# Optimization experiments

Hardware: AMD Instinct MI355X
Metric: run time of the kernel (lower is better)

The kernel has to match this reference:

```python
import jax, jax.numpy as jnp
import numpy as np

ALPHA = 0.2  # LeakyReLU negative slope
NEG_INF = -9e15


def setup_inputs() -> dict:
    key = jax.random.key(0)
    k1, k2, k3, k4 = jax.random.split(key, 4)
    B, N, F_in, F_out = 8, 2048, 256, 128
    h = jax.random.normal(k1, (B, N, F_in), dtype=jnp.float32)
    adj = jax.random.randint(k2, (B, N, N), 0, 2, dtype=jnp.int32)
    # xavier_uniform with gain=1.414
    def xavier(k, shape, gain=1.414):
        fan_in, fan_out = shape[0], shape[1]
        limit = gain * np.sqrt(6.0 / (fan_in + fan_out))
        return jax.random.uniform(k, shape, jnp.float32, -limit, limit)
    W = xavier(k3, (F_in, F_out))
    a = xavier(k4, (2 * F_out, 1))
    return {"h": h, "adj": adj, "W": W, "a": a}


def reference(h, adj, W, a):
    # h: [B,N,F_in], adj: [B,N,N], W: [F_in,F_out], a: [2*F_out,1]
    Wh = jnp.einsum('bnf,fe->bne', h, W)  # [B,N,E]
    E = Wh.shape[-1]
    a_src, a_dst = a[:E, 0], a[E:, 0]
    # e[b,i,j] = leakyrelu(Wh[b,i].a_src + Wh[b,j].a_dst)  (additive decomposition
    # of a @ concat(Wh_i, Wh_j) -- same math, no [B,N,N,2E] intermediate)
    s_src = Wh @ a_src  # [B,N]
    s_dst = Wh @ a_dst  # [B,N]
    e = jax.nn.leaky_relu(s_src[:, :, None] + s_dst[:, None, :], negative_slope=ALPHA)
    e = jnp.where(adj > 0, e, NEG_INF)
    attention = jax.nn.softmax(e, axis=2)  # [B,N,N]
    # dropout p=0.0 / eval mode -> identity
    h_prime = jnp.einsum('bij,bje->bie', attention, Wh)
    return jax.nn.elu(h_prime)  # concat=True
```

## Files before the change

kernel.cpp:

```cpp
#include <hip/hip_runtime.h>
#include <hip/hip_bf16.h>

#define GAT_ALPHA 0.2f
#define LOG2E 1.4426950408889634f

typedef float f32x4 __attribute__((ext_vector_type(4)));
typedef int   i32x4 __attribute__((ext_vector_type(4)));
typedef short bf16x8 __attribute__((ext_vector_type(8)));

static constexpr int Nn  = 2048;
static constexpr int FIN = 256;
static constexpr int FO  = 128;

static __device__ __forceinline__ unsigned short f2bf(float x) {
    __hip_bfloat16 h = __float2bfloat16(x);
    return __builtin_bit_cast(unsigned short, h);
}
static __device__ __forceinline__ float bf2f(unsigned short u) {
    unsigned int v = ((unsigned int)u) << 16;
    return __builtin_bit_cast(float, v);
}

__global__ __launch_bounds__(256) void gat_prep(
        const float* __restrict__ W, const float* __restrict__ a,
        float* __restrict__ wa, unsigned int* __restrict__ md_key)
{
    __shared__ float pr[32][8];
    __shared__ float pd[32][8];
    const int t = threadIdx.x;
    const int kl = t >> 3, seg = t & 7;
    const int k = blockIdx.x * 32 + kl;
    float ps = 0.f, pv = 0.f;
    const float* wr = W + (size_t)k * FO + seg * 16;
    #pragma unroll
    for (int f = 0; f < 16; f += 4) {
        f32x4 wv = *(const f32x4*)(wr + f);
        f32x4 as = *(const f32x4*)(a + seg * 16 + f);
        f32x4 ad = *(const f32x4*)(a + FO + seg * 16 + f);
        ps += wv[0]*as[0] + wv[1]*as[1] + wv[2]*as[2] + wv[3]*as[3];
        pv += wv[0]*ad[0] + wv[1]*ad[1] + wv[2]*ad[2] + wv[3]*ad[3];
    }
    pr[kl][seg] = ps; pd[kl][seg] = pv;
    __syncthreads();
    if (t < 32) {
        float s = 0.f, d = 0.f;
        #pragma unroll
        for (int j = 0; j < 8; ++j) { s += pr[t][j]; d += pd[t][j]; }
        wa[blockIdx.x * 32 + t]       = s;
        wa[256 + blockIdx.x * 32 + t] = d;
    }
    if (blockIdx.x == 0 && t < 8) md_key[t] = 0u;
}

__global__ __launch_bounds__(256) void gat_pack(
        const int* __restrict__ adj, unsigned int* __restrict__ mask)
{
    const int t = threadIdx.x, lane = t & 63, w = t >> 6;
    const size_t ibase = ((size_t)blockIdx.x * 4 + w) * 2048;
    const int* src = adj + ibase + lane;
    unsigned int myword = 0;
    #pragma unroll
    for (int c = 0; c < 32; ++c) {
        int v = src[(size_t)c * 64];
        unsigned long long m = __ballot(v > 0);
        if (lane == 2 * c)     myword = (unsigned int)m;
        if (lane == 2 * c + 1) myword = (unsigned int)(m >> 32);
    }
    mask[ibase / 32 + lane] = myword;
}

__global__ __launch_bounds__(256) void gat_wh(
        const float* __restrict__ h, const float* __restrict__ W,
        const float* __restrict__ wa, unsigned short* __restrict__ Wp,
        float* __restrict__ s_src, float* __restrict__ s_dst,
        unsigned int* __restrict__ md_key)
{
    __shared__ unsigned short WT[FO][264];
    __shared__ float wal[512];
    __shared__ float sred[64][4][2];
    __shared__ float red64[64];
    const int t  = threadIdx.x;
    const int b  = blockIdx.x & 7;
    const int n0 = (blockIdx.x >> 3) << 6;

    if (t < 128) *(f32x4*)&wal[t * 4] = *(const f32x4*)&wa[t * 4];
    #pragma unroll
    for (int c = 0; c < 32; ++c) {
        int flat = c * 1024 + t * 4;
        int k = flat >> 7, f = flat & 127;
        f32x4 wv = *(const f32x4*)&W[flat];
        WT[f + 0][k] = f2bf(wv[0]);
        WT[f + 1][k] = f2bf(wv[1]);
        WT[f + 2][k] = f2bf(wv[2]);
        WT[f + 3][k] = f2bf(wv[3]);
    }
    __syncthreads();

    {
        const int row = t >> 2, seg = t & 3;
        const float* hp  = h + ((size_t)(b * Nn + n0 + row)) * FIN + seg * 64;
        const float* was = &wal[seg * 64];
        const float* wad = &wal[256 + seg * 64];
        float ps = 0.f, pv = 0.f;
        #pragma unroll
        for (int j = 0; j < 64; j += 4) {
            f32x4 hv = *(const f32x4*)(hp + j);
            f32x4 sv = *(const f32x4*)(was + j);
            f32x4 dv = *(const f32x4*)(wad + j);
            ps += hv[0]*sv[0] + hv[1]*sv[1] + hv[2]*sv[2] + hv[3]*sv[3];
            pv += hv[0]*dv[0] + hv[1]*dv[1] + hv[2]*dv[2] + hv[3]*dv[3];
        }
        sred[row][seg][0] = ps;
        sred[row][seg][1] = pv;
    }
    __syncthreads();
    if (t < 64) {
        float s = sred[t][0][0] + sred[t][1][0] + sred[t][2][0] + sred[t][3][0];
        float d = sred[t][0][1] + sred[t][1][1] + sred[t][2][1] + sred[t][3][1];
        s_src[b * Nn + n0 + t] = s;
        s_dst[b * Nn + n0 + t] = d;
        red64[t] = d;
    }
    __syncthreads();
    if (t < 16) red64[t] = fmaxf(fmaxf(red64[t], red64[t + 16]),
                                 fmaxf(red64[t + 32], red64[t + 48]));
    __syncthreads();
    if (t == 0) {
        float m = red64[0];
        #pragma unroll
        for (int j = 1; j < 16; ++j) m = fmaxf(m, red64[j]);
        unsigned int bits = __builtin_bit_cast(unsigned int, m);
        unsigned int key  = (bits & 0x80000000u) ? ~bits : (bits | 0x80000000u);
        atomicMax(md_key + b, key);
    }

    const int w = t >> 6, lane = t & 63, n16 = lane & 15, quad = lane >> 4;
    const float* ha = h + ((size_t)(b * Nn + n0 + w * 16 + n16)) * FIN + quad * 8;
    f32x4 acc[8] = {};
    #pragma unroll
    for (int ks = 0; ks < 8; ++ks) {
        f32x4 h0 = *(const f32x4*)(ha + ks * 32);
        f32x4 h1 = *(const f32x4*)(ha + ks * 32 + 4);
        bf16x8 af;
        af[0] = (short)f2bf(h0[0]); af[1] = (short)f2bf(h0[1]);
        af[2] = (short)f2bf(h0[2]); af[3] = (short)f2bf(h0[3]);
        af[4] = (short)f2bf(h1[0]); af[5] = (short)f2bf(h1[1]);
        af[6] = (short)f2bf(h1[2]); af[7] = (short)f2bf(h1[3]);
        #pragma unroll
        for (int nt = 0; nt < 8; ++nt) {
            bf16x8 bfr = *(const bf16x8*)&WT[nt * 16 + n16][ks * 32 + quad * 8];
            acc[nt] = __builtin_amdgcn_mfma_f32_16x16x32_bf16(af, bfr, acc[nt], 0, 0, 0);
        }
    }
    {
        const int v      = (n0 >> 5) + (w >> 1);
        const int quad_p = ((w & 1) << 1) + (quad >> 1);
        const int eoff   = (quad & 1) << 2;
        #pragma unroll
        for (int nt = 0; nt < 8; ++nt) {
            ushort4 pk;
            pk.x = f2bf(acc[nt][0]); pk.y = f2bf(acc[nt][1]);
            pk.z = f2bf(acc[nt][2]); pk.w = f2bf(acc[nt][3]);
            size_t idx = ((((size_t)(b << 6) + v) * 8 + nt) * 64 + quad_p * 16 + n16) * 8 + eoff;
            *(ushort4*)&Wp[idx] = pk;
        }
    }
}

__global__ __launch_bounds__(512, 2) void gat_attn(
        const unsigned int* __restrict__ mask, const unsigned short* __restrict__ Wp,
        const float* __restrict__ s_src, const float* __restrict__ s_dst,
        const unsigned int* __restrict__ md_key, float* __restrict__ out)
{
    constexpr int AS = 132;
    constexpr int MS = 68;
    __shared__ __align__(16) float smem_f[64 * AS];
    __shared__ __align__(16) unsigned int mlds[64 * MS];
    __shared__ __align__(16) float dlds[Nn];
    __shared__ float l_red[64];
    unsigned short* ldsw = (unsigned short*)smem_f;

    const int t = threadIdx.x, w = t >> 6, lane = t & 63;
    const int n16 = lane & 15, quad = lane >> 4;
    const int rg = w & 3, jwin = w >> 2;
    const int b  = blockIdx.x & 7;
    const int i0 = (blockIdx.x >> 3) << 6;

    if (t < 64) l_red[t] = 0.f;

    {
        const unsigned int* msrc = mask + ((size_t)(b * Nn + i0)) * 64 + t * 8;
        i32x4 m0 = *(const i32x4*)(msrc);
        i32x4 m1 = *(const i32x4*)(msrc + 4);
        const int r = t >> 3, wd = (t & 7) * 8;
        *(i32x4*)&mlds[r * MS + wd]     = m0;
        *(i32x4*)&mlds[r * MS + wd + 4] = m1;
    }
    {
        f32x4 dv = *(const f32x4*)(s_dst + b * Nn + t * 4);
        *(f32x4*)&dlds[t * 4] = dv;
    }

    const unsigned int key = md_key[b];
    const unsigned int mb  = (key & 0x80000000u) ? (key ^ 0x80000000u) : ~key;
    const float mdb = __builtin_bit_cast(float, mb);

    const int row = i0 + rg * 16 + n16;
    const float ssr = s_src[b * Nn + row];
    const float tm  = ssr + mdb;
    const float mi  = fmaxf(tm, GAT_ALPHA * tm) * LOG2E;
    const float sL  = ssr * LOG2E;

    const int jw = (jwin << 5) + (quad << 3);
    const int mrow = (rg * 16 + n16) * MS;
    const unsigned short* wsrc = Wp + ((size_t)b << 18) + (t << 4);

    f32x4 acc[8] = {};
    float ls = 0.f;

    {
        f32x4 g0 = *(const f32x4*)(wsrc);
        f32x4 g1 = *(const f32x4*)(wsrc + 8);
        *(f32x4*)&ldsw[(t << 4)]     = g0;
        *(f32x4*)&ldsw[(t << 4) + 8] = g1;
    }
    __syncthreads();

    for (int s = 0; s < 32; ++s) {
        const int j0  = s << 6;
        const int cur = s & 1, nxt = cur ^ 1;
        const unsigned int mword = mlds[mrow + s * 2 + jwin];
        const unsigned int mbyte = (mword >> (quad * 8)) & 0xffu;
        f32x4 d0 = *(const f32x4*)&dlds[j0 + jw];
        f32x4 d1 = *(const f32x4*)&dlds[j0 + jw + 4];
        f32x4 g0, g1;
        if (s < 31) {
            const unsigned short* src = wsrc + (size_t)(s + 1) * 8192;
            g0 = *(const f32x4*)(src);
            g1 = *(const f32x4*)(src + 8);
        }

        bf16x8 af;
        #pragma unroll
        for (int j = 0; j < 4; ++j) {
            float u  = __builtin_fmaf(d0[j], LOG2E, sL);
            float lr = fmaxf(u, GAT_ALPHA * u);
            float e  = __builtin_amdgcn_exp2f(lr - mi);
            e = ((mbyte >> j) & 1u) ? e : 0.f;
            unsigned short us = f2bf(e);
            ls += bf2f(us); af[j] = (short)us;
        }
        #pragma unroll
        for (int j = 0; j < 4; ++j) {
            float u  = __builtin_fmaf(d1[j], LOG2E, sL);
            float lr = fmaxf(u, GAT_ALPHA * u);
            float e  = __builtin_amdgcn_exp2f(lr - mi);
            e = ((mbyte >> (4 + j)) & 1u) ? e : 0.f;
            unsigned short us = f2bf(e);
            ls += bf2f(us); af[4 + j] = (short)us;
        }

        const unsigned short* bbase = &ldsw[cur * 8192 + (jwin << 12) + (lane << 3)];
        #pragma unroll
        for (int nt = 0; nt < 8; ++nt) {
            bf16x8 bfr = *(const bf16x8*)(bbase + (nt << 9));
            acc[nt] = __builtin_amdgcn_mfma_f32_16x16x32_bf16(af, bfr, acc[nt], 0, 0, 0);
        }

        if (s < 31) {
            *(f32x4*)&ldsw[nxt * 8192 + (t << 4)]     = g0;
            *(f32x4*)&ldsw[nxt * 8192 + (t << 4) + 8] = g1;
        }
        __syncthreads();
    }

    ls += __shfl_xor(ls, 16); ls += __shfl_xor(ls, 32);
    if (quad == 0) atomicAdd(&l_red[rg * 16 + n16], ls);

    float* slotp = smem_f + (size_t)(rg * 16) * AS;
    if (jwin == 0) {
        #pragma unroll
        for (int nt = 0; nt < 8; ++nt)
            #pragma unroll
            for (int rr = 0; rr < 4; ++rr)
                slotp[(quad * 4 + rr) * AS + nt * 16 + n16] = acc[nt][rr];
    }
    __syncthreads();
    if (jwin == 1) {
        #pragma unroll
        for (int nt = 0; nt < 8; ++nt)
            #pragma unroll
            for (int rr = 0; rr < 4; ++rr)
                slotp[(quad * 4 + rr) * AS + nt * 16 + n16] += acc[nt][rr];
    }
    __syncthreads();

    float* ob = out + ((size_t)(b * Nn + i0)) * FO;
    #pragma unroll
    for (int c = 0; c < 4; ++c) {
        int flat = c * 2048 + t * 4;
        int m = flat >> 7, f = flat & 127;
        f32x4 v = *(const f32x4*)&smem_f[(size_t)m * AS + f];
        float l = l_red[m];
        f32x4 o;
        #pragma unroll
        for (int j = 0; j < 4; ++j) {
            float x = v[j] / l;
            o[j] = x > 0.f ? x : expm1f(x);
        }
        *(f32x4*)&ob[(size_t)m * FO + f] = o;
    }
}

extern "C" void kernel_launch(void* const* d_in, const int* in_sizes, int n_in,
                              void* d_out, int out_size, void* d_ws, size_t ws_size,
                              hipStream_t stream)
{
    const float* h   = (const float*)d_in[0];
    const int*   adj = (const int*)d_in[1];
    const float* W   = (const float*)d_in[2];
    const float* a   = (const float*)d_in[3];
    float* out = (float*)d_out;

    char* ws = (char*)d_ws;
    unsigned short* Wp  = (unsigned short*)ws;
    float* s_src        = (float*)(ws + 4194304);
    float* s_dst        = (float*)(ws + 4259840);
    float* wa           = (float*)(ws + 4325376);
    unsigned int* md_key= (unsigned int*)(ws + 4327424);
    unsigned int* mask  = (unsigned int*)(ws + 8388608);

    hipLaunchKernelGGL(gat_prep, dim3(8),    dim3(256), 0, stream, W, a, wa, md_key);
    hipLaunchKernelGGL(gat_wh,   dim3(256),  dim3(256), 0, stream, h, W, wa, Wp, s_src, s_dst, md_key);
    hipLaunchKernelGGL(gat_pack, dim3(4096), dim3(256), 0, stream, adj, mask);
    hipLaunchKernelGGL(gat_attn, dim3(256),  dim3(512), 0, stream, mask, Wp, s_src, s_dst, md_key, out);
}
```

Before: 247.5 us.

## Give each wave two row groups over 128-column tiles with deeper prefetch

Each wave now computes two 16-row groups against 32-column windows of a 128-column j-tile, so every LDS B-fragment feeds two MFMAs. Wh tiles are prefetched two steps ahead through rotating register buffers, in a loop unrolled by two with an explicit waitcnt and barrier. The cross-window reduction now uses two partial-sum LDS slabs summed in the epilogue, and the mask LDS pitch changes to 65 to avoid bank conflicts. The aim is fewer LDS reads and barriers per unit of work and better latency hiding. The cost is higher register and LDS use, which drops occupancy to one block per CU.

```diff
diff --git a/kernel.cpp b/kernel.cpp
--- a/kernel.cpp
+++ b/kernel.cpp
@@ -167,14 +167,14 @@
     }
 }
 
-__global__ __launch_bounds__(512, 2) void gat_attn(
+__global__ __launch_bounds__(512, 1) void gat_attn(
         const unsigned int* __restrict__ mask, const unsigned short* __restrict__ Wp,
         const float* __restrict__ s_src, const float* __restrict__ s_dst,
         const unsigned int* __restrict__ md_key, float* __restrict__ out)
 {
     constexpr int AS = 132;
-    constexpr int MS = 68;
-    __shared__ __align__(16) float smem_f[64 * AS];
+    constexpr int MS = 65;
+    __shared__ __align__(16) float smem_f[2 * 64 * AS];
     __shared__ __align__(16) unsigned int mlds[64 * MS];
     __shared__ __align__(16) float dlds[Nn];
     __shared__ float l_red[64];
@@ -182,116 +182,149 @@
 
     const int t = threadIdx.x, w = t >> 6, lane = t & 63;
     const int n16 = lane & 15, quad = lane >> 4;
-    const int rg = w & 3, jwin = w >> 2;
+    const int rg = w & 1, jwin = w >> 1;
     const int b  = blockIdx.x & 7;
     const int i0 = (blockIdx.x >> 3) << 6;
 
     if (t < 64) l_red[t] = 0.f;
 
+    const unsigned short* wsrc = Wp + ((size_t)b << 18);
+
+    f32x4 g0[4], gA[4], gB[4];
+    #pragma unroll
+    for (int p = 0; p < 4; ++p) g0[p] = *(const f32x4*)(wsrc + p * 4096 + t * 8);
+    #pragma unroll
+    for (int p = 0; p < 4; ++p) gA[p] = *(const f32x4*)(wsrc + 16384 + p * 4096 + t * 8);
+    i32x4 m0, m1;
     {
         const unsigned int* msrc = mask + ((size_t)(b * Nn + i0)) * 64 + t * 8;
-        i32x4 m0 = *(const i32x4*)(msrc);
-        i32x4 m1 = *(const i32x4*)(msrc + 4);
-        const int r = t >> 3, wd = (t & 7) * 8;
-        *(i32x4*)&mlds[r * MS + wd]     = m0;
-        *(i32x4*)&mlds[r * MS + wd + 4] = m1;
-    }
+        m0 = *(const i32x4*)(msrc);
+        m1 = *(const i32x4*)(msrc + 4);
+    }
+    f32x4 dv = *(const f32x4*)(s_dst + b * Nn + t * 4);
+
+    const unsigned int key = md_key[b];
+    const unsigned int mb_ = (key & 0x80000000u) ? (key ^ 0x80000000u) : ~key;
+    const float mdb = __builtin_bit_cast(float, mb_);
+    const int r0 = i0 + rg * 32 + n16;
+    const float ssr0 = s_src[b * Nn + r0];
+    const float ssr1 = s_src[b * Nn + r0 + 16];
+    const float tm0 = ssr0 + mdb, tm1 = ssr1 + mdb;
+    const float mi0 = fmaxf(tm0, GAT_ALPHA * tm0) * LOG2E;
+    const float mi1 = fmaxf(tm1, GAT_ALPHA * tm1) * LOG2E;
+    const float sL0 = ssr0 * LOG2E, sL1 = ssr1 * LOG2E;
+    const int jw = (jwin << 5) + (quad << 3);
+    const int mrow0 = (rg * 32 + n16) * MS;
+    const int mrow1 = mrow0 + 16 * MS;
+
+    #pragma unroll
+    for (int p = 0; p < 4; ++p) *(f32x4*)&ldsw[p * 4096 + t * 8] = g0[p];
     {
-        f32x4 dv = *(const f32x4*)(s_dst + b * Nn + t * 4);
-        *(f32x4*)&dlds[t * 4] = dv;
-    }
-
-    const unsigned int key = md_key[b];
-    const unsigned int mb  = (key & 0x80000000u) ? (key ^ 0x80000000u) : ~key;
-    const float mdb = __builtin_bit_cast(float, mb);
-
-    const int row = i0 + rg * 16 + n16;
-    const float ssr = s_src[b * Nn + row];
-    const float tm  = ssr + mdb;
-    const float mi  = fmaxf(tm, GAT_ALPHA * tm) * LOG2E;
-    const float sL  = ssr * LOG2E;
-
-    const int jw = (jwin << 5) + (quad << 3);
-    const int mrow = (rg * 16 + n16) * MS;
-    const unsigned short* wsrc = Wp + ((size_t)b << 18) + (t << 4);
-
-    f32x4 acc[8] = {};
-    float ls = 0.f;
-
-    {
-        f32x4 g0 = *(const f32x4*)(wsrc);
-        f32x4 g1 = *(const f32x4*)(wsrc + 8);
-        *(f32x4*)&ldsw[(t << 4)]     = g0;
-        *(f32x4*)&ldsw[(t << 4) + 8] = g1;
-    }
-    __syncthreads();
-
-    for (int s = 0; s < 32; ++s) {
-        const int j0  = s << 6;
-        const int cur = s & 1, nxt = cur ^ 1;
-        const unsigned int mword = mlds[mrow + s * 2 + jwin];
-        const unsigned int mbyte = (mword >> (quad * 8)) & 0xffu;
-        f32x4 d0 = *(const f32x4*)&dlds[j0 + jw];
-        f32x4 d1 = *(const f32x4*)&dlds[j0 + jw + 4];
-        f32x4 g0, g1;
-        if (s < 31) {
-            const unsigned short* src = wsrc + (size_t)(s + 1) * 8192;
-            g0 = *(const f32x4*)(src);
-            g1 = *(const f32x4*)(src + 8);
-        }
-
-        bf16x8 af;
-        #pragma unroll
-        for (int j = 0; j < 4; ++j) {
-            float u  = __builtin_fmaf(d0[j], LOG2E, sL);
-            float lr = fmaxf(u, GAT_ALPHA * u);
-            float e  = __builtin_amdgcn_exp2f(lr - mi);
-            e = ((mbyte >> j) & 1u) ? e : 0.f;
-            unsigned short us = f2bf(e);
-            ls += bf2f(us); af[j] = (short)us;
-        }
-        #pragma unroll
-        for (int j = 0; j < 4; ++j) {
-            float u  = __builtin_fmaf(d1[j], LOG2E, sL);
-            float lr = fmaxf(u, GAT_ALPHA * u);
-            float e  = __builtin_amdgcn_exp2f(lr - mi);
-            e = ((mbyte >> (4 + j)) & 1u) ? e : 0.f;
-            unsigned short us = f2bf(e);
-            ls += bf2f(us); af[4 + j] = (short)us;
-        }
-
-        const unsigned short* bbase = &ldsw[cur * 8192 + (jwin << 12) + (lane << 3)];
-        #pragma unroll
-        for (int nt = 0; nt < 8; ++nt) {
-            bf16x8 bfr = *(const bf16x8*)(bbase + (nt << 9));
-            acc[nt] = __builtin_amdgcn_mfma_f32_16x16x32_bf16(af, bfr, acc[nt], 0, 0, 0);
-        }
-
-        if (s < 31) {
-            *(f32x4*)&ldsw[nxt * 8192 + (t << 4)]     = g0;
-            *(f32x4*)&ldsw[nxt * 8192 + (t << 4) + 8] = g1;
-        }
-        __syncthreads();
-    }
-
-    ls += __shfl_xor(ls, 16); ls += __shfl_xor(ls, 32);
-    if (quad == 0) atomicAdd(&l_red[rg * 16 + n16], ls);
-
-    float* slotp = smem_f + (size_t)(rg * 16) * AS;
-    if (jwin == 0) {
-        #pragma unroll
-        for (int nt = 0; nt < 8; ++nt)
+        const int r = t >> 3, c8 = (t & 7) * 8;
+        *(i32x4*)&mlds[r * MS + c8]     = m0;
+        *(i32x4*)&mlds[r * MS + c8 + 4] = m1;
+    }
+    *(f32x4*)&dlds[t * 4] = dv;
+
+    f32x4 acc[2][8] = {};
+    float ls0 = 0.f, ls1 = 0.f;
+    __syncthreads();
+
+#define GAT_TILE(S, CUR, GP, GN)                                                \
+    {                                                                           \
+        const int s_ = (S);                                                     \
+        const int j0 = s_ << 7;                                                 \
+           \
+        if (s_ < 14) {                                                          \
+            const unsigned short* src = wsrc + (size_t)(s_ + 2) * 16384;        \
+            _Pragma("unroll")                                                   \
+            for (int p = 0; p < 4; ++p)                                         \
+                GN[p] = *(const f32x4*)(src + p * 4096 + t * 8);                \
+        }                                                                       \
+        const unsigned int mw0 = mlds[mrow0 + (s_ << 2) + jwin];                \
+        const unsigned int mw1 = mlds[mrow1 + (s_ << 2) + jwin];                \
+        const unsigned int mb0 = (mw0 >> (quad << 3)) & 0xffu;                  \
+        const unsigned int mb1 = (mw1 >> (quad << 3)) & 0xffu;                  \
+        f32x4 d0 = *(const f32x4*)&dlds[j0 + jw];                               \
+        f32x4 d1 = *(const f32x4*)&dlds[j0 + jw + 4];                           \
+        bf16x8 af0, af1;                                                        \
+        _Pragma("unroll")                                                       \
+        for (int j = 0; j < 4; ++j) {                                           \
+            {   float u  = __builtin_fmaf(d0[j], LOG2E, sL0);                   \
+                float lr = fmaxf(u, GAT_ALPHA * u);                             \
+                float e  = __builtin_amdgcn_exp2f(lr - mi0);                    \
+                e = ((mb0 >> j) & 1u) ? e : 0.f;                                \
+                unsigned short us = f2bf(e);                                    \
+                ls0 += bf2f(us); af0[j] = (short)us; }                          \
+            {   float u  = __builtin_fmaf(d1[j], LOG2E, sL0);                   \
+                float lr = fmaxf(u, GAT_ALPHA * u);                             \
+                float e  = __builtin_amdgcn_exp2f(lr - mi0);                    \
+                e = ((mb0 >> (4 + j)) & 1u) ? e : 0.f;                          \
+                unsigned short us = f2bf(e);                                    \
+                ls0 += bf2f(us); af0[4 + j] = (short)us; }                      \
+            {   float u  = __builtin_fmaf(d0[j], LOG2E, sL1);                   \
+                float lr = fmaxf(u, GAT_ALPHA * u);                             \
+                float e  = __builtin_amdgcn_exp2f(lr - mi1);                    \
+                e = ((mb1 >> j) & 1u) ? e : 0.f;                                \
+                unsigned short us = f2bf(e);                                    \
+                ls1 += bf2f(us); af1[j] = (short)us; }                          \
+            {   float u  = __builtin_fmaf(d1[j], LOG2E, sL1);                   \
+                float lr = fmaxf(u, GAT_ALPHA * u);                             \
+                float e  = __builtin_amdgcn_exp2f(lr - mi1);                    \
+                e = ((mb1 >> (4 + j)) & 1u) ? e : 0.f;                          \
+                unsigned short us = f2bf(e);                                    \
+                ls1 += bf2f(us); af1[4 + j] = (short)us; }                      \
+        }                                                                       \
+        const unsigned short* bbase = &ldsw[(CUR) * 16384 + (jwin << 12) + (lane << 3)]; \
+        _Pragma("unroll")                                                       \
+        for (int nt = 0; nt < 8; ++nt) {                                        \
+            bf16x8 bfr = *(const bf16x8*)(bbase + (nt << 9));                   \
+            acc[0][nt] = __builtin_amdgcn_mfma_f32_16x16x32_bf16(af0, bfr, acc[0][nt], 0, 0, 0); \
+            acc[1][nt] = __builtin_amdgcn_mfma_f32_16x16x32_bf16(af1, bfr, acc[1][nt], 0, 0, 0); \
+        }                                                                       \
+              \
+        if (s_ < 15) {                                                          \
+            _Pragma("unroll")                                                   \
+            for (int p = 0; p < 4; ++p)                                         \
+                *(f32x4*)&ldsw[((CUR) ^ 1) * 16384 + p * 4096 + t * 8] = GP[p]; \
+        }                                                                       \
+        asm volatile("s_waitcnt lgkmcnt(0)" ::: "memory");                      \
+        __builtin_amdgcn_s_barrier();                                           \
+    }
+
+    for (int s = 0; s < 16; s += 2) {
+        GAT_TILE(s,     0, gA, gB)
+        GAT_TILE(s + 1, 1, gB, gA)
+    }
+#undef GAT_TILE
+
+    ls0 += __shfl_xor(ls0, 16); ls0 += __shfl_xor(ls0, 32);
+    ls1 += __shfl_xor(ls1, 16); ls1 += __shfl_xor(ls1, 32);
+    if (quad == 0) {
+        atomicAdd(&l_red[rg * 32 + n16], ls0);
+        atomicAdd(&l_red[rg * 32 + 16 + n16], ls1);
+    }
+
+    float* slot = smem_f + (size_t)(jwin & 1) * (64 * AS);
+    const int rbase = rg * 32;
+    if (jwin < 2) {
+        #pragma unroll
+        for (int ig = 0; ig < 2; ++ig)
             #pragma unroll
-            for (int rr = 0; rr < 4; ++rr)
-                slotp[(quad * 4 + rr) * AS + nt * 16 + n16] = acc[nt][rr];
-    }
-    __syncthreads();
-    if (jwin == 1) {
-        #pragma unroll
-        for (int nt = 0; nt < 8; ++nt)
+            for (int nt = 0; nt < 8; ++nt)
+                #pragma unroll
+                for (int rr = 0; rr < 4; ++rr)
+                    slot[(size_t)(rbase + ig * 16 + quad * 4 + rr) * AS + nt * 16 + n16] = acc[ig][nt][rr];
+    }
+    __syncthreads();
+    if (jwin >= 2) {
+        #pragma unroll
+        for (int ig = 0; ig < 2; ++ig)
             #pragma unroll
-            for (int rr = 0; rr < 4; ++rr)
-                slotp[(quad * 4 + rr) * AS + nt * 16 + n16] += acc[nt][rr];
+            for (int nt = 0; nt < 8; ++nt)
+                #pragma unroll
+                for (int rr = 0; rr < 4; ++rr)
+                    slot[(size_t)(rbase + ig * 16 + quad * 4 + rr) * AS + nt * 16 + n16] += acc[ig][nt][rr];
     }
     __syncthreads();
 
@@ -300,12 +333,13 @@
     for (int c = 0; c < 4; ++c) {
         int flat = c * 2048 + t * 4;
         int m = flat >> 7, f = flat & 127;
-        f32x4 v = *(const f32x4*)&smem_f[(size_t)m * AS + f];
+        f32x4 v0 = *(const f32x4*)&smem_f[(size_t)m * AS + f];
+        f32x4 v1 = *(const f32x4*)&smem_f[(size_t)(64 + m) * AS + f];
         float l = l_red[m];
         f32x4 o;
         #pragma unroll
         for (int j = 0; j < 4; ++j) {
-            float x = v[j] / l;
+            float x = (v0[j] + v1[j]) / l;
             o[j] = x > 0.f ? x : expm1f(x);
         }
         *(f32x4*)&ob[(size_t)m * FO + f] = o;
```

After: 247.0 us. About the same (-0.2%).
